# Kernel optimization log

Measured on AMD Instinct MI355X. Metric: run time of the kernel, lower is better.

## Reference

```python
import jax, jax.numpy as jnp
import numpy as np

EPS = 1e-12  # matches F.normalize default eps

def _angle(e):
    # e: [N, D] embeddings
    d = e[:, None, :] - e[None, :, :]                      # [N, N, D] pairwise differences
    n = jnp.linalg.norm(d, axis=-1, keepdims=True)         # [N, N, 1]
    d = d / jnp.maximum(n, EPS)                            # normalized diffs; diagonal stays 0
    # all-triplet cosines: for each anchor i, Gram matrix of its normalized diffs
    return jnp.einsum('ijd,ikd->ijk', d, d)                # [N, N, N]

def _smooth_l1_mean(a, b):
    # torch F.smooth_l1_loss with beta=1.0, reduction='mean'
    x = jnp.abs(a - b)
    return jnp.mean(jnp.where(x < 1.0, 0.5 * x * x, x - 0.5))

def setup_inputs() -> dict:
    key = jax.random.key(0)
    k1, k2 = jax.random.split(key)
    student = jax.random.normal(k1, (384, 256), dtype=jnp.float32)
    teacher = jax.random.normal(k2, (384, 256), dtype=jnp.float32)
    return {"student": student, "teacher": teacher}

def reference(student, teacher):
    s_angle = _angle(student)
    t_angle = _angle(teacher)
    return _smooth_l1_mean(s_angle, t_angle)
```

## Files before the change

kernel.cpp:

```cpp
#include <hip/hip_runtime.h>
#include <hip/hip_bf16.h>

#define NPTS 384
#define DIMS 256
#define TI 4
#define JC 48

__global__ void gram_kernel(const float* __restrict__ Es, const float* __restrict__ Et,
                            float* __restrict__ Gs, float* __restrict__ Gt) {
    const float* __restrict__ E = (blockIdx.z == 0) ? Es : Et;
    float* __restrict__ G       = (blockIdx.z == 0) ? Gs : Gt;

    __shared__ float As[32][33];
    __shared__ float Bs[32][33];

    const int tx = threadIdx.x;
    const int ty = threadIdx.y;
    const int t  = ty * 16 + tx;
    const int lr = t >> 5;
    const int lc = t & 31;
    const int i0 = blockIdx.x * 32;
    const int j0 = blockIdx.y * 32;

    float acc00 = 0.f, acc01 = 0.f, acc10 = 0.f, acc11 = 0.f;

    for (int k0 = 0; k0 < DIMS; k0 += 32) {
#pragma unroll
        for (int rr = 0; rr < 4; rr++) {
            As[lr + 8 * rr][lc] = E[(i0 + lr + 8 * rr) * DIMS + k0 + lc];
            Bs[lr + 8 * rr][lc] = E[(j0 + lr + 8 * rr) * DIMS + k0 + lc];
        }
        __syncthreads();
#pragma unroll
        for (int k = 0; k < 32; k++) {
            float a0 = As[2 * ty][k], a1 = As[2 * ty + 1][k];
            float b0 = Bs[2 * tx][k], b1 = Bs[2 * tx + 1][k];
            acc00 = fmaf(a0, b0, acc00);
            acc01 = fmaf(a0, b1, acc01);
            acc10 = fmaf(a1, b0, acc10);
            acc11 = fmaf(a1, b1, acc11);
        }
        __syncthreads();
    }

    const int i = i0 + 2 * ty;
    const int j = j0 + 2 * tx;
    G[i * NPTS + j]           = acc00;
    G[i * NPTS + j + 1]       = acc01;
    G[(i + 1) * NPTS + j]     = acc10;
    G[(i + 1) * NPTS + j + 1] = acc11;
}

__global__ void invnorm_kernel(const float* __restrict__ Gs, const float* __restrict__ Gt,
                               float* __restrict__ Rs, float* __restrict__ Rt) {
    const float* __restrict__ G = (blockIdx.y == 0) ? Gs : Gt;
    float* __restrict__ R       = (blockIdx.y == 0) ? Rs : Rt;

    int idx = blockIdx.x * 256 + threadIdx.x;
    if (idx >= NPTS * NPTS) return;
    int i = idx / NPTS;
    int j = idx - i * NPTS;

    float gii = G[i * NPTS + i];
    float gjj = G[j * NPTS + j];
    float v   = gii - 2.0f * G[idx] + gjj;
    float n   = sqrtf(fmaxf(v, 0.0f));
    float r   = 1.0f / fmaxf(n, 1e-12f);
    R[idx] = (i == j) ? 0.0f : r;
}

__global__ __launch_bounds__(NPTS) void rkd_angle_kernel(
        const float* __restrict__ Gs, const float* __restrict__ Gt,
        const float* __restrict__ Rs, const float* __restrict__ Rt,
        float* __restrict__ out) {
    __shared__ float sGs[TI][NPTS];
    __shared__ float sGt[TI][NPTS];
    __shared__ float sRs[TI][NPTS];
    __shared__ float sRt[TI][NPTS];

    const int tid = threadIdx.x;
    const int i0  = blockIdx.x * TI;
    const int j0  = blockIdx.y * JC;

#pragma unroll
    for (int r = 0; r < TI; r++) {
        int row = (i0 + r) * NPTS;
        sGs[r][tid] = Gs[row + tid];
        sGt[r][tid] = Gt[row + tid];
        sRs[r][tid] = Rs[row + tid];
        sRt[r][tid] = Rt[row + tid];
    }
    __syncthreads();

    const int k = tid;
    float gii_s[TI], gii_t[TI], rik_s[TI], rik_t[TI], qik_s[TI], qik_t[TI];
#pragma unroll
    for (int r = 0; r < TI; r++) {
        gii_s[r] = sGs[r][i0 + r];
        gii_t[r] = sGt[r][i0 + r];
        rik_s[r] = sRs[r][k];
        rik_t[r] = sRt[r][k];
        qik_s[r] = rik_s[r] * sGs[r][k];
        qik_t[r] = rik_t[r] * sGt[r][k];
    }

    float acc = 0.0f;
    for (int j = j0; j < j0 + JC; j++) {
        float gs_jk = Gs[j * NPTS + k];
        float gt_jk = Gt[j * NPTS + k];
#pragma unroll
        for (int r = 0; r < TI; r++) {
            float cs = gii_s[r] - sGs[r][j];
            float as = sRs[r][j] * fmaf(rik_s[r], gs_jk + cs, -qik_s[r]);
            float ct = gii_t[r] - sGt[r][j];
            float at = sRt[r][j] * fmaf(rik_t[r], gt_jk + ct, -qik_t[r]);
            float x  = fabsf(as - at);
            acc += (x < 1.0f) ? 0.5f * x * x : x - 0.5f;
        }
    }

#pragma unroll
    for (int off = 32; off > 0; off >>= 1)
        acc += __shfl_down(acc, off, 64);

    __shared__ float wsum[NPTS / 64];
    const int wid  = tid >> 6;
    const int lane = tid & 63;
    if (lane == 0) wsum[wid] = acc;
    __syncthreads();
    if (tid == 0) {
        float s = 0.0f;
#pragma unroll
        for (int w = 0; w < NPTS / 64; w++) s += wsum[w];
        atomicAdd(out, s * (1.0f / (384.0f * 384.0f * 384.0f)));
    }
}

extern "C" void kernel_launch(void* const* d_in, const int* in_sizes, int n_in,
                              void* d_out, int out_size, void* d_ws, size_t ws_size,
                              hipStream_t stream) {
    const float* student = (const float*)d_in[0];
    const float* teacher = (const float*)d_in[1];
    float* out = (float*)d_out;

    float* Gs = (float*)d_ws;
    float* Gt = Gs + NPTS * NPTS;
    float* Rs = Gt + NPTS * NPTS;
    float* Rt = Rs + NPTS * NPTS;

    hipMemsetAsync(d_out, 0, sizeof(float), stream);

    dim3 ggrid(NPTS / 32, NPTS / 32, 2);
    dim3 gblock(16, 16, 1);
    gram_kernel<<<ggrid, gblock, 0, stream>>>(student, teacher, Gs, Gt);

    dim3 ngrid((NPTS * NPTS + 255) / 256, 2, 1);
    invnorm_kernel<<<ngrid, 256, 0, stream>>>(Gs, Gt, Rs, Rt);

    dim3 mgrid(NPTS / TI, NPTS / JC, 1);
    rkd_angle_kernel<<<mgrid, NPTS, 0, stream>>>(Gs, Gt, Rs, Rt, out);
}
```

Before: 102.0 us.

## Pack Gram and inverse-norm data into interleaved float4/float2 arrays, retile gram kernel

The Gram kernel now uses 64-thread blocks, each computing a 4x4 register tile with float4 global loads and transposed shared memory. The separate inverse-norm kernel is replaced by a pack kernel that writes interleaved float4 (gii-gij, r_s, tii-tij, r_t) and float2 (gs, gt) records, so the main kernel fetches student and teacher values in one vector load. The main kernel drops its shared-memory staging and reads row-i data straight from global/cache. It also halves JC to double the grid and uses a branchless smooth-L1 form. The cost is larger workspace traffic (24 bytes per pair) and more redundant global loads of P[j] inside the inner loop.

```diff
diff --git a/kernel.cpp b/kernel.cpp
--- a/kernel.cpp
+++ b/kernel.cpp
@@ -1,121 +1,117 @@
 #include <hip/hip_runtime.h>
-#include <hip/hip_bf16.h>
 
 #define NPTS 384
 #define DIMS 256
 #define TI 4
-#define JC 48
+#define JC 24
 
-__global__ void gram_kernel(const float* __restrict__ Es, const float* __restrict__ Et,
-                            float* __restrict__ Gs, float* __restrict__ Gt) {
+__global__ __launch_bounds__(64) void gram_kernel(const float* __restrict__ Es,
+                                                  const float* __restrict__ Et,
+                                                  float* __restrict__ Gs,
+                                                  float* __restrict__ Gt) {
     const float* __restrict__ E = (blockIdx.z == 0) ? Es : Et;
     float* __restrict__ G       = (blockIdx.z == 0) ? Gs : Gt;
 
-    __shared__ float As[32][33];
-    __shared__ float Bs[32][33];
+    __shared__ float AsT[32][36];
+    __shared__ float BsT[32][36];
 
-    const int tx = threadIdx.x;
-    const int ty = threadIdx.y;
-    const int t  = ty * 16 + tx;
-    const int lr = t >> 5;
-    const int lc = t & 31;
+    const int t  = threadIdx.x;
+    const int tx = t & 7;
+    const int ty = t >> 3;
     const int i0 = blockIdx.x * 32;
     const int j0 = blockIdx.y * 32;
 
-    float acc00 = 0.f, acc01 = 0.f, acc10 = 0.f, acc11 = 0.f;
+    float acc[4][4] = {};
 
     for (int k0 = 0; k0 < DIMS; k0 += 32) {
 #pragma unroll
-        for (int rr = 0; rr < 4; rr++) {
-            As[lr + 8 * rr][lc] = E[(i0 + lr + 8 * rr) * DIMS + k0 + lc];
-            Bs[lr + 8 * rr][lc] = E[(j0 + lr + 8 * rr) * DIMS + k0 + lc];
+        for (int m = 0; m < 4; m++) {
+            const int row = ty + 8 * m;
+            float va[4], vb[4];
+            *(float4*)va = *(const float4*)&E[(i0 + row) * DIMS + k0 + 4 * tx];
+            *(float4*)vb = *(const float4*)&E[(j0 + row) * DIMS + k0 + 4 * tx];
+#pragma unroll
+            for (int q = 0; q < 4; q++) {
+                AsT[4 * tx + q][row] = va[q];
+                BsT[4 * tx + q][row] = vb[q];
+            }
         }
         __syncthreads();
 #pragma unroll
         for (int k = 0; k < 32; k++) {
-            float a0 = As[2 * ty][k], a1 = As[2 * ty + 1][k];
-            float b0 = Bs[2 * tx][k], b1 = Bs[2 * tx + 1][k];
-            acc00 = fmaf(a0, b0, acc00);
-            acc01 = fmaf(a0, b1, acc01);
-            acc10 = fmaf(a1, b0, acc10);
-            acc11 = fmaf(a1, b1, acc11);
+            float a[4], b[4];
+            *(float4*)a = *(const float4*)&AsT[k][4 * ty];
+            *(float4*)b = *(const float4*)&BsT[k][4 * tx];
+#pragma unroll
+            for (int p = 0; p < 4; p++)
+#pragma unroll
+                for (int q = 0; q < 4; q++)
+                    acc[p][q] = fmaf(a[p], b[q], acc[p][q]);
         }
         __syncthreads();
     }
 
-    const int i = i0 + 2 * ty;
-    const int j = j0 + 2 * tx;
-    G[i * NPTS + j]           = acc00;
-    G[i * NPTS + j + 1]       = acc01;
-    G[(i + 1) * NPTS + j]     = acc10;
-    G[(i + 1) * NPTS + j + 1] = acc11;
+#pragma unroll
+    for (int p = 0; p < 4; p++) {
+        float4 v = make_float4(acc[p][0], acc[p][1], acc[p][2], acc[p][3]);
+        *(float4*)&G[(i0 + 4 * ty + p) * NPTS + j0 + 4 * tx] = v;
+    }
 }
 
-__global__ void invnorm_kernel(const float* __restrict__ Gs, const float* __restrict__ Gt,
-                               float* __restrict__ Rs, float* __restrict__ Rt) {
-    const float* __restrict__ G = (blockIdx.y == 0) ? Gs : Gt;
-    float* __restrict__ R       = (blockIdx.y == 0) ? Rs : Rt;
-
+__global__ void pack_kernel(const float* __restrict__ Gs, const float* __restrict__ Gt,
+                            float4* __restrict__ P, float2* __restrict__ W) {
     int idx = blockIdx.x * 256 + threadIdx.x;
     if (idx >= NPTS * NPTS) return;
     int i = idx / NPTS;
     int j = idx - i * NPTS;
 
-    float gii = G[i * NPTS + i];
-    float gjj = G[j * NPTS + j];
-    float v   = gii - 2.0f * G[idx] + gjj;
-    float n   = sqrtf(fmaxf(v, 0.0f));
-    float r   = 1.0f / fmaxf(n, 1e-12f);
-    R[idx] = (i == j) ? 0.0f : r;
+    float gs   = Gs[idx];
+    float gt   = Gt[idx];
+    float gsii = Gs[i * (NPTS + 1)];
+    float gsjj = Gs[j * (NPTS + 1)];
+    float gtii = Gt[i * (NPTS + 1)];
+    float gtjj = Gt[j * (NPTS + 1)];
+
+    float vs = fmaxf(gsii - 2.0f * gs + gsjj, 0.0f);
+    float vt = fmaxf(gtii - 2.0f * gt + gtjj, 0.0f);
+    float rs = (i == j) ? 0.0f : 1.0f / fmaxf(sqrtf(vs), 1e-12f);
+    float rt = (i == j) ? 0.0f : 1.0f / fmaxf(sqrtf(vt), 1e-12f);
+
+    P[idx] = make_float4(gsii - gs, rs, gtii - gt, rt);
+    W[idx] = make_float2(gs, gt);
 }
 
 __global__ __launch_bounds__(NPTS) void rkd_angle_kernel(
-        const float* __restrict__ Gs, const float* __restrict__ Gt,
-        const float* __restrict__ Rs, const float* __restrict__ Rt,
+        const float4* __restrict__ P, const float2* __restrict__ W,
         float* __restrict__ out) {
-    __shared__ float sGs[TI][NPTS];
-    __shared__ float sGt[TI][NPTS];
-    __shared__ float sRs[TI][NPTS];
-    __shared__ float sRt[TI][NPTS];
+    const int k  = threadIdx.x;
+    const int i0 = blockIdx.x * TI;
+    const int j0 = blockIdx.y * JC;
 
-    const int tid = threadIdx.x;
-    const int i0  = blockIdx.x * TI;
-    const int j0  = blockIdx.y * JC;
-
+    float rsk[TI], rtk[TI], nqs[TI], nqt[TI];
 #pragma unroll
     for (int r = 0; r < TI; r++) {
-        int row = (i0 + r) * NPTS;
-        sGs[r][tid] = Gs[row + tid];
-        sGt[r][tid] = Gt[row + tid];
-        sRs[r][tid] = Rs[row + tid];
-        sRt[r][tid] = Rt[row + tid];
-    }
-    __syncthreads();
-
-    const int k = tid;
-    float gii_s[TI], gii_t[TI], rik_s[TI], rik_t[TI], qik_s[TI], qik_t[TI];
-#pragma unroll
-    for (int r = 0; r < TI; r++) {
-        gii_s[r] = sGs[r][i0 + r];
-        gii_t[r] = sGt[r][i0 + r];
-        rik_s[r] = sRs[r][k];
-        rik_t[r] = sRt[r][k];
-        qik_s[r] = rik_s[r] * sGs[r][k];
-        qik_t[r] = rik_t[r] * sGt[r][k];
+        float4 pk = P[(i0 + r) * NPTS + k];
+        float2 wk = W[(i0 + r) * NPTS + k];
+        rsk[r] = pk.y;
+        rtk[r] = pk.w;
+        nqs[r] = -(pk.y * wk.x);
+        nqt[r] = -(pk.w * wk.y);
     }
 
     float acc = 0.0f;
+#pragma unroll 4
     for (int j = j0; j < j0 + JC; j++) {
-        float gs_jk = Gs[j * NPTS + k];
-        float gt_jk = Gt[j * NPTS + k];
+        float2 w = W[j * NPTS + k];
 #pragma unroll
         for (int r = 0; r < TI; r++) {
-            float cs = gii_s[r] - sGs[r][j];
-            float as = sRs[r][j] * fmaf(rik_s[r], gs_jk + cs, -qik_s[r]);
-            float ct = gii_t[r] - sGt[r][j];
-            float at = sRt[r][j] * fmaf(rik_t[r], gt_jk + ct, -qik_t[r]);
-            float x  = fabsf(as - at);
-            acc += (x < 1.0f) ? 0.5f * x * x : x - 0.5f;
+            float4 pj = P[(i0 + r) * NPTS + j];
+            float as = pj.y * fmaf(rsk[r], w.x + pj.x, nqs[r]);
+            float at = pj.w * fmaf(rtk[r], w.y + pj.z, nqt[r]);
+            float d  = as - at;
+            float ad = fabsf(d);
+            float m  = fminf(ad, 1.0f);
+            acc = fmaf(m, fmaf(-0.5f, m, ad), acc);
         }
     }
 
@@ -124,11 +120,11 @@
         acc += __shfl_down(acc, off, 64);
 
     __shared__ float wsum[NPTS / 64];
-    const int wid  = tid >> 6;
-    const int lane = tid & 63;
+    const int wid  = k >> 6;
+    const int lane = k & 63;
     if (lane == 0) wsum[wid] = acc;
     __syncthreads();
-    if (tid == 0) {
+    if (k == 0) {
         float s = 0.0f;
 #pragma unroll
         for (int w = 0; w < NPTS / 64; w++) s += wsum[w];
@@ -143,20 +139,19 @@
     const float* teacher = (const float*)d_in[1];
     float* out = (float*)d_out;
 
-    float* Gs = (float*)d_ws;
-    float* Gt = Gs + NPTS * NPTS;
-    float* Rs = Gt + NPTS * NPTS;
-    float* Rt = Rs + NPTS * NPTS;
+    float4* P  = (float4*)d_ws;
+    float2* W  = (float2*)(P + NPTS * NPTS);
+    float*  Gs = (float*)(W + NPTS * NPTS);
+    float*  Gt = Gs + NPTS * NPTS;
 
     hipMemsetAsync(d_out, 0, sizeof(float), stream);
 
     dim3 ggrid(NPTS / 32, NPTS / 32, 2);
-    dim3 gblock(16, 16, 1);
-    gram_kernel<<<ggrid, gblock, 0, stream>>>(student, teacher, Gs, Gt);
+    gram_kernel<<<ggrid, 64, 0, stream>>>(student, teacher, Gs, Gt);
 
-    dim3 ngrid((NPTS * NPTS + 255) / 256, 2, 1);
-    invnorm_kernel<<<ngrid, 256, 0, stream>>>(Gs, Gt, Rs, Rt);
+    dim3 pgrid((NPTS * NPTS + 255) / 256, 1, 1);
+    pack_kernel<<<pgrid, 256, 0, stream>>>(Gs, Gt, P, W);
 
     dim3 mgrid(NPTS / TI, NPTS / JC, 1);
-    rkd_angle_kernel<<<mgrid, NPTS, 0, stream>>>(Gs, Gt, Rs, Rt, out);
+    rkd_angle_kernel<<<mgrid, NPTS, 0, stream>>>(P, W, out);
 }
```

Result: no change. 101.8 us (-0.2%).
